# Kernel optimization log

Hardware: AMD Instinct MI355X
Metric: run time of the kernel (lower is better)

Reference implementation:

```python
import jax, jax.numpy as jnp
import numpy as np

B, S, D_IN, D_OUT = 4, 4096, 2048, 2048
DELTA_A = 0.0
DELTA_W = 0.05


def setup_inputs() -> dict:
    key = jax.random.key(0)
    kx, kw = jax.random.split(key)
    # xavier_uniform bound for [out, in] weight
    bound = float(np.sqrt(6.0 / (D_IN + D_OUT)))
    x = jax.random.normal(kx, (B, S, D_IN), dtype=jnp.float32)
    W = jax.random.uniform(kw, (D_OUT, D_IN), dtype=jnp.float32, minval=-bound, maxval=bound)
    b = jnp.zeros((D_OUT,), dtype=jnp.float32)
    return {"x": x, "W": W, "b": b}


def reference(x, W, b):
    # --- activation ternarization (BitNet STE); pre_ln=False -> identity ---
    ax = jnp.abs(x)
    thr_a = DELTA_A * jnp.mean(ax, axis=-1, keepdims=True)
    xa = jnp.where(ax < thr_a, jnp.zeros_like(x), jnp.sign(x))
    x_final = x + jax.lax.stop_gradient(xa - x)

    # --- weight ternarization with per-row alpha scale ---
    Wc = W - jnp.mean(W, axis=1, keepdims=True)
    aWc = jnp.abs(Wc)
    thr_w = DELTA_W * jnp.mean(aWc, axis=1, keepdims=True)
    code = jnp.where(aWc < thr_w, jnp.zeros_like(Wc), jnp.sign(Wc))
    nz = (code != 0).astype(Wc.dtype)
    alpha = jnp.sum(aWc * nz, axis=1, keepdims=True) / jnp.clip(
        jnp.sum(nz, axis=1, keepdims=True), 1.0, None
    )
    Wq = alpha * code
    W_final = W + jax.lax.stop_gradient(Wq - W)

    # F.linear: y = x @ W^T + b
    return jnp.einsum("bsd,od->bso", x_final, W_final) + b
```

## Files before the change

### kernel.cpp

```cpp
#include <hip/hip_runtime.h>
#include <stdint.h>

#define K_DIM   2048
#define N_DIM   2048
#define M_DIM   16384
#define DELTA_W 0.05f

#define BM 128
#define BN 128
#define BK 128

typedef __attribute__((ext_vector_type(4))) int i32x4;

__device__ __forceinline__ void async_copy16(const void* g, void* l) {
    __builtin_amdgcn_global_load_lds(
        (__attribute__((address_space(1))) void*)g,
        (__attribute__((address_space(3))) void*)l,
        16, 0, 0);
}

__device__ __forceinline__ float block_sum_256(float v, float* sm) {
#pragma unroll
    for (int o = 32; o > 0; o >>= 1) v += __shfl_down(v, o, 64);
    const int lane = threadIdx.x & 63;
    const int w    = threadIdx.x >> 6;
    __syncthreads();
    if (lane == 0) sm[w] = v;
    __syncthreads();
    return sm[0] + sm[1] + sm[2] + sm[3];
}

__global__ __launch_bounds__(256) void quant_kernel(
    const float* __restrict__ W, const float* __restrict__ x,
    int8_t* __restrict__ code, float* __restrict__ alpha,
    int8_t* __restrict__ xq)
{
    __shared__ float sm[4];
    const int t = threadIdx.x;

    if (blockIdx.x < N_DIM) {
        const int row = blockIdx.x;
        const float* Wr = W + (size_t)row * K_DIM;

        float v[8];
        float s = 0.f;
#pragma unroll
        for (int i = 0; i < 8; ++i) { v[i] = Wr[t + i * 256]; s += v[i]; }
        const float mean = block_sum_256(s, sm) * (1.0f / K_DIM);

        float sa = 0.f;
#pragma unroll
        for (int i = 0; i < 8; ++i) sa += fabsf(v[i] - mean);
        const float thr = DELTA_W * (block_sum_256(sa, sm) * (1.0f / K_DIM));

        float ssum = 0.f, scnt = 0.f;
        int8_t q[8];
#pragma unroll
        for (int i = 0; i < 8; ++i) {
            const float c = v[i] - mean;
            const float a = fabsf(c);
            int8_t qv = 0;
            if (a >= thr) qv = (int8_t)((c > 0.f) - (c < 0.f));
            q[i] = qv;
            if (qv != 0) { ssum += a; scnt += 1.0f; }
        }
        const float num = block_sum_256(ssum, sm);
        const float den = block_sum_256(scnt, sm);
        if (t == 0) alpha[row] = num / fmaxf(den, 1.0f);

#pragma unroll
        for (int i = 0; i < 8; ++i)
            code[(size_t)row * K_DIM + t + i * 256] = q[i];
    } else {
        const int blk = blockIdx.x - N_DIM;
        const int base = blk * 1024 + t;
        const float4* xin = (const float4*)x;
        char4* xo = (char4*)xq;
#pragma unroll
        for (int i = 0; i < 4; ++i) {
            const float4 f = xin[base + i * 256];
            char4 c;
            c.x = (char)((f.x > 0.f) - (f.x < 0.f));
            c.y = (char)((f.y > 0.f) - (f.y < 0.f));
            c.z = (char)((f.z > 0.f) - (f.z < 0.f));
            c.w = (char)((f.w > 0.f) - (f.w < 0.f));
            xo[base + i * 256] = c;
        }
    }
}

__global__ __launch_bounds__(256) void gemm_kernel(
    const int8_t* __restrict__ A, const int8_t* __restrict__ Bt,
    const float* __restrict__ alpha, const float* __restrict__ bias,
    float* __restrict__ out)
{
    __shared__ __align__(16) int8_t As[BM * BK];
    __shared__ __align__(16) int8_t Bs[BN * BK];

    const int tid  = threadIdx.x;
    const int lane = tid & 63;
    const int wv   = tid >> 6;
    const int wm   = (wv >> 1) * 64;
    const int wn   = (wv & 1) * 64;

    const int tileM = blockIdx.y * BM;
    const int tileN = blockIdx.x * BN;

    i32x4 acc[4][4] = {};

    const int8_t* aptr[4];
    const int8_t* bptr[4];
#pragma unroll
    for (int e = 0; e < 4; ++e) {
        const int slot = e * 256 + tid;
        const int r    = slot >> 3;
        const int cg   = (slot & 7) ^ (r & 7);
        aptr[e] = A  + (size_t)(tileM + r) * K_DIM + cg * 16;
        bptr[e] = Bt + (size_t)(tileN + r) * K_DIM + cg * 16;
    }

    const int fr = lane & 15;
    const int q  = lane >> 4;

    for (int k0 = 0; k0 < K_DIM; k0 += BK) {
#pragma unroll
        for (int e = 0; e < 4; ++e) {
            async_copy16(aptr[e] + k0, &As[(e * 256 + tid) * 16]);
            async_copy16(bptr[e] + k0, &Bs[(e * 256 + tid) * 16]);
        }
        __syncthreads();

#pragma unroll
        for (int kk = 0; kk < 2; ++kk) {
            i32x4 af[4], bf[4];
#pragma unroll
            for (int i = 0; i < 4; ++i) {
                const int m  = wm + i * 16 + fr;
                const int cs = (kk * 4 + q) ^ (m & 7);
                af[i] = *(const i32x4*)&As[m * BK + cs * 16];
            }
#pragma unroll
            for (int j = 0; j < 4; ++j) {
                const int n  = wn + j * 16 + fr;
                const int cs = (kk * 4 + q) ^ (n & 7);
                bf[j] = *(const i32x4*)&Bs[n * BK + cs * 16];
            }
#pragma unroll
            for (int i = 0; i < 4; ++i)
#pragma unroll
                for (int j = 0; j < 4; ++j)
                    acc[i][j] = __builtin_amdgcn_mfma_i32_16x16x64_i8(
                        af[i], bf[j], acc[i][j], 0, 0, 0);
        }
        __syncthreads();
    }

    const int cl = lane & 15;
    const int qr = lane >> 4;
#pragma unroll
    for (int j = 0; j < 4; ++j) {
        const int n  = tileN + wn + j * 16 + cl;
        const float al = alpha[n];
        const float bi = bias[n];
#pragma unroll
        for (int i = 0; i < 4; ++i) {
            const int mbase = tileM + wm + i * 16 + qr * 4;
#pragma unroll
            for (int r = 0; r < 4; ++r) {
                out[(size_t)(mbase + r) * N_DIM + n] =
                    al * (float)acc[i][j][r] + bi;
            }
        }
    }
}

extern "C" void kernel_launch(void* const* d_in, const int* in_sizes, int n_in,
                              void* d_out, int out_size, void* d_ws, size_t ws_size,
                              hipStream_t stream) {
    const float* x = (const float*)d_in[0];
    const float* W = (const float*)d_in[1];
    const float* b = (const float*)d_in[2];
    float* out = (float*)d_out;

    int8_t* xq    = (int8_t*)d_ws;
    int8_t* wcode = xq + (size_t)M_DIM * K_DIM;
    float*  alpha = (float*)(wcode + (size_t)N_DIM * K_DIM);

    quant_kernel<<<N_DIM + 8192, 256, 0, stream>>>(W, x, wcode, alpha, xq);

    dim3 grid(N_DIM / BN, M_DIM / BM);
    gemm_kernel<<<grid, dim3(256), 0, stream>>>(xq, wcode, alpha, b, out);
}
```

Baseline: 307.1 us.

## Enlarge GEMM tile to 256x256 with 512 threads and double-buffered LDS prefetch

```diff
diff --git a/kernel.cpp b/kernel.cpp
--- a/kernel.cpp
+++ b/kernel.cpp
@@ -6,9 +6,10 @@
 #define M_DIM   16384
 #define DELTA_W 0.05f
 
-#define BM 128
-#define BN 128
+#define BM 256
+#define BN 256
 #define BK 128
+#define NT (K_DIM / BK)
 
 typedef __attribute__((ext_vector_type(4))) int i32x4;
 
@@ -89,71 +90,132 @@
     }
 }
 
-__global__ __launch_bounds__(256) void gemm_kernel(
+__global__ __launch_bounds__(512) void gemm_kernel(
     const int8_t* __restrict__ A, const int8_t* __restrict__ Bt,
     const float* __restrict__ alpha, const float* __restrict__ bias,
     float* __restrict__ out)
 {
-    __shared__ __align__(16) int8_t As[BM * BK];
-    __shared__ __align__(16) int8_t Bs[BN * BK];
+    __shared__ __align__(16) int8_t As[2][BM * BK];
+    __shared__ __align__(16) int8_t Bs[2][BN * BK];
 
     const int tid  = threadIdx.x;
     const int lane = tid & 63;
     const int wv   = tid >> 6;
-    const int wm   = (wv >> 1) * 64;
-    const int wn   = (wv & 1) * 64;
+    const int wm   = (wv >> 2) * 128;
+    const int wn   = (wv & 3) * 64;
+    const int fr   = lane & 15;
+    const int q    = lane >> 4;
+    const int c0   = q ^ (fr & 7);
 
     const int tileM = blockIdx.y * BM;
     const int tileN = blockIdx.x * BN;
 
-    i32x4 acc[4][4] = {};
-
-    const int8_t* aptr[4];
-    const int8_t* bptr[4];
-#pragma unroll
-    for (int e = 0; e < 4; ++e) {
-        const int slot = e * 256 + tid;
-        const int r    = slot >> 3;
-        const int cg   = (slot & 7) ^ (r & 7);
-        aptr[e] = A  + (size_t)(tileM + r) * K_DIM + cg * 16;
-        bptr[e] = Bt + (size_t)(tileN + r) * K_DIM + cg * 16;
-    }
-
-    const int fr = lane & 15;
-    const int q  = lane >> 4;
-
-    for (int k0 = 0; k0 < K_DIM; k0 += BK) {
-#pragma unroll
-        for (int e = 0; e < 4; ++e) {
-            async_copy16(aptr[e] + k0, &As[(e * 256 + tid) * 16]);
-            async_copy16(bptr[e] + k0, &Bs[(e * 256 + tid) * 16]);
-        }
-        __syncthreads();
-
-#pragma unroll
-        for (int kk = 0; kk < 2; ++kk) {
-            i32x4 af[4], bf[4];
-#pragma unroll
-            for (int i = 0; i < 4; ++i) {
-                const int m  = wm + i * 16 + fr;
-                const int cs = (kk * 4 + q) ^ (m & 7);
-                af[i] = *(const i32x4*)&As[m * BK + cs * 16];
-            }
-#pragma unroll
-            for (int j = 0; j < 4; ++j) {
-                const int n  = wn + j * 16 + fr;
-                const int cs = (kk * 4 + q) ^ (n & 7);
-                bf[j] = *(const i32x4*)&Bs[n * BK + cs * 16];
-            }
-#pragma unroll
-            for (int i = 0; i < 4; ++i)
-#pragma unroll
-                for (int j = 0; j < 4; ++j)
-                    acc[i][j] = __builtin_amdgcn_mfma_i32_16x16x64_i8(
-                        af[i], bf[j], acc[i][j], 0, 0, 0);
-        }
-        __syncthreads();
-    }
+    size_t a_src[2][2], b_src[2][2];
+#pragma unroll
+    for (int e = 0; e < 2; ++e) {
+        const int s  = e * 512 + tid;
+        const int r  = s >> 3;
+        const int cg = (s & 7) ^ (r & 7);
+#pragma unroll
+        for (int h = 0; h < 2; ++h) {
+            a_src[h][e] = (size_t)(tileM + h * 128 + r) * K_DIM + cg * 16;
+            b_src[h][e] = (size_t)(tileN + h * 128 + r) * K_DIM + cg * 16;
+        }
+    }
+
+    i32x4 acc[8][4] = {};
+    i32x4 af[2][4], bf0[2][2], bf1[2][2];
+
+#define STAGE_A(nbp, h, kk0) do {                                              \
+    async_copy16(A  + a_src[h][0] + (kk0), &As[nbp][(h) * 16384 + tid * 16]);  \
+    async_copy16(A  + a_src[h][1] + (kk0),                                     \
+                 &As[nbp][(h) * 16384 + 8192 + tid * 16]);                     \
+} while (0)
+#define STAGE_B(nbp, h, kk0) do {                                              \
+    async_copy16(Bt + b_src[h][0] + (kk0), &Bs[nbp][(h) * 16384 + tid * 16]);  \
+    async_copy16(Bt + b_src[h][1] + (kk0),                                     \
+                 &Bs[nbp][(h) * 16384 + 8192 + tid * 16]);                     \
+} while (0)
+
+    STAGE_A(0, 0, 0); STAGE_B(0, 0, 0);
+    STAGE_B(0, 1, 0); STAGE_A(0, 1, 0);
+
+    int k1 = 0;
+
+#define GROUP(bp, DS, WV) {                                                    \
+    const int8_t* Ac = As[(bp)];                                               \
+    const int8_t* Bc = Bs[(bp)];                                               \
+    const int nb = (bp) ^ 1;                                                   \
+    if (DS) { STAGE_A(nb, 0, k1); STAGE_B(nb, 0, k1);                          \
+              STAGE_B(nb, 1, k1); STAGE_A(nb, 1, k1); }                        \
+    asm volatile("s_waitcnt vmcnt(" WV ")\n\ts_barrier" ::: "memory");         \
+                               \
+    _Pragma("unroll")                                                          \
+    for (int i = 0; i < 4; ++i) {                                              \
+        const int r8 = (wm + i * 16 + fr) * 128;                               \
+        af[0][i] = *(const i32x4*)(Ac + r8 + c0 * 16);                         \
+        af[1][i] = *(const i32x4*)(Ac + r8 + (c0 ^ 4) * 16);                   \
+    }                                                                          \
+    _Pragma("unroll")                                                          \
+    for (int j = 0; j < 2; ++j) {                                              \
+        const int r8a = (wn + j * 16 + fr) * 128;                              \
+        bf0[0][j] = *(const i32x4*)(Bc + r8a + c0 * 16);                       \
+        bf0[1][j] = *(const i32x4*)(Bc + r8a + (c0 ^ 4) * 16);                 \
+        const int r8b = (wn + 32 + j * 16 + fr) * 128;                         \
+        bf1[0][j] = *(const i32x4*)(Bc + r8b + c0 * 16);                       \
+        bf1[1][j] = *(const i32x4*)(Bc + r8b + (c0 ^ 4) * 16);                 \
+    }                                                                          \
+                                    \
+    _Pragma("unroll")                                                          \
+    for (int i = 0; i < 4; ++i) {                                              \
+        _Pragma("unroll")                                                      \
+        for (int j = 0; j < 2; ++j) {                                          \
+            acc[i][j] = __builtin_amdgcn_mfma_i32_16x16x64_i8(                 \
+                af[0][i], bf0[0][j], acc[i][j], 0, 0, 0);                      \
+            acc[i][j] = __builtin_amdgcn_mfma_i32_16x16x64_i8(                 \
+                af[1][i], bf0[1][j], acc[i][j], 0, 0, 0);                      \
+            acc[i][j + 2] = __builtin_amdgcn_mfma_i32_16x16x64_i8(             \
+                af[0][i], bf1[0][j], acc[i][j + 2], 0, 0, 0);                  \
+            acc[i][j + 2] = __builtin_amdgcn_mfma_i32_16x16x64_i8(             \
+                af[1][i], bf1[1][j], acc[i][j + 2], 0, 0, 0);                  \
+        }                                                                      \
+    }                                                                          \
+                      \
+    _Pragma("unroll")                                                          \
+    for (int i = 0; i < 4; ++i) {                                              \
+        const int r8 = (wm + 64 + i * 16 + fr) * 128;                          \
+        af[0][i] = *(const i32x4*)(Ac + r8 + c0 * 16);                         \
+        af[1][i] = *(const i32x4*)(Ac + r8 + (c0 ^ 4) * 16);                   \
+    }                                                                          \
+                                    \
+    _Pragma("unroll")                                                          \
+    for (int i = 0; i < 4; ++i) {                                              \
+        _Pragma("unroll")                                                      \
+        for (int j = 0; j < 2; ++j) {                                          \
+            acc[i + 4][j] = __builtin_amdgcn_mfma_i32_16x16x64_i8(             \
+                af[0][i], bf0[0][j], acc[i + 4][j], 0, 0, 0);                  \
+            acc[i + 4][j] = __builtin_amdgcn_mfma_i32_16x16x64_i8(             \
+                af[1][i], bf0[1][j], acc[i + 4][j], 0, 0, 0);                  \
+            acc[i + 4][j + 2] = __builtin_amdgcn_mfma_i32_16x16x64_i8(         \
+                af[0][i], bf1[0][j], acc[i + 4][j + 2], 0, 0, 0);              \
+            acc[i + 4][j + 2] = __builtin_amdgcn_mfma_i32_16x16x64_i8(         \
+                af[1][i], bf1[1][j], acc[i + 4][j + 2], 0, 0, 0);              \
+        }                                                                      \
+    }                                                                          \
+                    \
+    asm volatile("s_barrier" ::: "memory");                                    \
+}
+
+#pragma unroll 1
+    for (int t = 0; t < NT - 1; ++t) {
+        k1 = (t + 1) * BK;
+        GROUP(t & 1, 1, "8");
+    }
+    GROUP((NT - 1) & 1, 0, "0");
+
+#undef GROUP
+#undef STAGE_A
+#undef STAGE_B
 
     const int cl = lane & 15;
     const int qr = lane >> 4;
@@ -163,7 +225,7 @@
         const float al = alpha[n];
         const float bi = bias[n];
 #pragma unroll
-        for (int i = 0; i < 4; ++i) {
+        for (int i = 0; i < 8; ++i) {
             const int mbase = tileM + wm + i * 16 + qr * 4;
 #pragma unroll
             for (int r = 0; r < 4; ++r) {
@@ -189,5 +251,5 @@
     quant_kernel<<<N_DIM + 8192, 256, 0, stream>>>(W, x, wcode, alpha, xq);
 
     dim3 grid(N_DIM / BN, M_DIM / BM);
-    gemm_kernel<<<grid, dim3(256), 0, stream>>>(xq, wcode, alpha, b, out);
-}
+    gemm_kernel<<<grid, dim3(512), 0, stream>>>(xq, wcode, alpha, b, out);
+}
```

Result: no change. 312.0 us (+1.6%).

## Double-buffer int8 GEMM with 128x256 tiles, 512 threads, XCD-aware block mapping

Applied to the files above, without the earlier changes.

```diff
diff --git a/kernel.cpp b/kernel.cpp
--- a/kernel.cpp
+++ b/kernel.cpp
@@ -7,8 +7,9 @@
 #define DELTA_W 0.05f
 
 #define BM 128
-#define BN 128
-#define BK 128
+#define BN 256
+#define BK 64
+#define NT (K_DIM / BK)
 
 typedef __attribute__((ext_vector_type(4))) int i32x4;
 
@@ -89,71 +90,84 @@
     }
 }
 
-__global__ __launch_bounds__(256) void gemm_kernel(
+__global__ __launch_bounds__(512, 4) void gemm_kernel(
     const int8_t* __restrict__ A, const int8_t* __restrict__ Bt,
     const float* __restrict__ alpha, const float* __restrict__ bias,
     float* __restrict__ out)
 {
-    __shared__ __align__(16) int8_t As[BM * BK];
-    __shared__ __align__(16) int8_t Bs[BN * BK];
+    __shared__ __align__(16) int8_t As[2][BM * BK];
+    __shared__ __align__(16) int8_t Bs[2][BN * BK];
 
     const int tid  = threadIdx.x;
     const int lane = tid & 63;
     const int wv   = tid >> 6;
-    const int wm   = (wv >> 1) * 64;
-    const int wn   = (wv & 1) * 64;
-
-    const int tileM = blockIdx.y * BM;
-    const int tileN = blockIdx.x * BN;
+    const int wm   = (wv >> 2) * 64;
+    const int wn   = (wv & 3) * 64;
+    const int fr   = lane & 15;
+    const int q    = lane >> 4;
+    const int cs16 = (q ^ ((fr >> 1) & 3)) * 16;
+
+    const int bid = blockIdx.x;
+    const int xcd = bid & 7;
+    const int idx = bid >> 3;
+    const int tileN = (idx & 7) * BN;
+    const int tileM = ((idx >> 3) + (xcd << 4)) * BM;
+
+    const int ra = tid >> 2;
+    const int ca = (tid & 3) ^ ((ra >> 1) & 3);
+    const unsigned a_off = (unsigned)(tileM + ra) * K_DIM + ca * 16;
+    unsigned b_off[2];
+#pragma unroll
+    for (int e = 0; e < 2; ++e) {
+        const int s  = e * 512 + tid;
+        const int rb = s >> 2;
+        const int cb = (s & 3) ^ ((rb >> 1) & 3);
+        b_off[e] = (unsigned)(tileN + rb) * K_DIM + cb * 16;
+    }
 
     i32x4 acc[4][4] = {};
-
-    const int8_t* aptr[4];
-    const int8_t* bptr[4];
-#pragma unroll
-    for (int e = 0; e < 4; ++e) {
-        const int slot = e * 256 + tid;
-        const int r    = slot >> 3;
-        const int cg   = (slot & 7) ^ (r & 7);
-        aptr[e] = A  + (size_t)(tileM + r) * K_DIM + cg * 16;
-        bptr[e] = Bt + (size_t)(tileN + r) * K_DIM + cg * 16;
-    }
-
-    const int fr = lane & 15;
-    const int q  = lane >> 4;
-
-    for (int k0 = 0; k0 < K_DIM; k0 += BK) {
-#pragma unroll
-        for (int e = 0; e < 4; ++e) {
-            async_copy16(aptr[e] + k0, &As[(e * 256 + tid) * 16]);
-            async_copy16(bptr[e] + k0, &Bs[(e * 256 + tid) * 16]);
-        }
-        __syncthreads();
-
-#pragma unroll
-        for (int kk = 0; kk < 2; ++kk) {
-            i32x4 af[4], bf[4];
-#pragma unroll
-            for (int i = 0; i < 4; ++i) {
-                const int m  = wm + i * 16 + fr;
-                const int cs = (kk * 4 + q) ^ (m & 7);
-                af[i] = *(const i32x4*)&As[m * BK + cs * 16];
-            }
-#pragma unroll
-            for (int j = 0; j < 4; ++j) {
-                const int n  = wn + j * 16 + fr;
-                const int cs = (kk * 4 + q) ^ (n & 7);
-                bf[j] = *(const i32x4*)&Bs[n * BK + cs * 16];
-            }
-#pragma unroll
-            for (int i = 0; i < 4; ++i)
-#pragma unroll
-                for (int j = 0; j < 4; ++j)
-                    acc[i][j] = __builtin_amdgcn_mfma_i32_16x16x64_i8(
-                        af[i], bf[j], acc[i][j], 0, 0, 0);
-        }
-        __syncthreads();
-    }
+    i32x4 af[4], bf[4];
+
+#define STAGE(nbp, kk0) do {                                                   \
+    async_copy16(A  + a_off    + (kk0), &As[nbp][tid * 16]);                   \
+    async_copy16(Bt + b_off[0] + (kk0), &Bs[nbp][tid * 16]);                   \
+    async_copy16(Bt + b_off[1] + (kk0), &Bs[nbp][8192 + tid * 16]);            \
+} while (0)
+
+    STAGE(0, 0);
+
+    int k1 = 0;
+
+#define GROUP(bp, DS, WV) {                                                    \
+    const int8_t* Ac = As[(bp)];                                               \
+    const int8_t* Bc = Bs[(bp)];                                               \
+    if (DS) { STAGE((bp) ^ 1, k1); }                                           \
+    asm volatile("s_waitcnt vmcnt(" WV ")\n\ts_barrier" ::: "memory");         \
+    _Pragma("unroll")                                                          \
+    for (int i = 0; i < 4; ++i)                                                \
+        af[i] = *(const i32x4*)(Ac + (wm + i * 16 + fr) * 64 + cs16);          \
+    _Pragma("unroll")                                                          \
+    for (int j = 0; j < 4; ++j)                                                \
+        bf[j] = *(const i32x4*)(Bc + (wn + j * 16 + fr) * 64 + cs16);          \
+    _Pragma("unroll")                                                          \
+    for (int i = 0; i < 4; ++i) {                                              \
+        _Pragma("unroll")                                                      \
+        for (int j = 0; j < 4; ++j)                                            \
+            acc[i][j] = __builtin_amdgcn_mfma_i32_16x16x64_i8(                 \
+                af[i], bf[j], acc[i][j], 0, 0, 0);                             \
+    }                                                                          \
+    asm volatile("s_barrier" ::: "memory");                                    \
+}
+
+#pragma unroll 1
+    for (int t = 0; t < NT - 1; ++t) {
+        k1 = (t + 1) * BK;
+        GROUP(t & 1, 1, "3");
+    }
+    GROUP((NT - 1) & 1, 0, "0");
+
+#undef GROUP
+#undef STAGE
 
     const int cl = lane & 15;
     const int qr = lane >> 4;
@@ -188,6 +202,5 @@
 
     quant_kernel<<<N_DIM + 8192, 256, 0, stream>>>(W, x, wcode, alpha, xq);
 
-    dim3 grid(N_DIM / BN, M_DIM / BM);
-    gemm_kernel<<<grid, dim3(256), 0, stream>>>(xq, wcode, alpha, b, out);
-}
+    gemm_kernel<<<1024, dim3(512), 0, stream>>>(xq, wcode, alpha, b, out);
+}
```

Measured after the change: 307.2 us. About the same (+0.1%).
